# Performance work log

Hardware: AMD Instinct MI355X
Metric: run time of the kernel (lower is better)

## Reference

```python
import jax, jax.numpy as jnp
import numpy as np

B, N, D, Z, H = 256, 128, 256, 64, 128

def setup_inputs() -> dict:
    key = jax.random.key(0)
    ks = jax.random.split(key, 12)
    s = 0.02
    inp = {
        "h_obs": jax.random.normal(ks[0], (B, N, D), jnp.float32),
        "z": jax.random.normal(ks[1], (B, N, Z), jnp.float32),
        "start_pos": jax.random.normal(ks[2], (B, N, 2), jnp.float32),
        # input_proj: Linear(D+Z+2 -> H)
        "W_in": jax.random.normal(ks[3], (D + Z + 2, H), jnp.float32) * s,
        "b_in": jax.random.normal(ks[4], (H,), jnp.float32) * s,
        # GRUCell weights, PyTorch layout: [3H, H] rows ordered (r, z, n)
        "W_ih": jax.random.normal(ks[5], (3 * H, H), jnp.float32) * s,
        "b_ih": jax.random.normal(ks[6], (3 * H,), jnp.float32) * s,
        "W_hh": jax.random.normal(ks[7], (3 * H, H), jnp.float32) * s,
        "b_hh": jax.random.normal(ks[8], (3 * H,), jnp.float32) * s,
        # out_proj: Linear(H -> 2)
        "W_out": jax.random.normal(ks[9], (2, H), jnp.float32) * s,
        "b_out": jax.random.normal(ks[10], (2,), jnp.float32) * s,
        "pred_len": 30,
    }
    return inp

def _gru_cell(x, h, W_ih, b_ih, W_hh, b_hh):
    gi = x @ W_ih.T + b_ih            # [BN, 3H]
    gh = h @ W_hh.T + b_hh            # [BN, 3H]
    i_r, i_z, i_n = jnp.split(gi, 3, axis=-1)
    h_r, h_z, h_n = jnp.split(gh, 3, axis=-1)
    r = jax.nn.sigmoid(i_r + h_r)
    zg = jax.nn.sigmoid(i_z + h_z)
    n = jnp.tanh(i_n + r * h_n)
    return (1.0 - zg) * n + zg * h

def reference(h_obs, z, start_pos, W_in, b_in, W_ih, b_ih, W_hh, b_hh, W_out, b_out, pred_len):
    BN = B * N
    # h_obs and z are constant across steps: precompute their projection once.
    base = jnp.concatenate([h_obs, z], axis=-1).reshape(BN, D + Z)
    base_proj = base @ W_in[: D + Z] + b_in            # [BN, H]
    W_pos = W_in[D + Z:]                               # [2, H]

    state0 = jnp.zeros((BN, H), h_obs.dtype)
    pos0 = start_pos.reshape(BN, 2)

    def step(carry, _):
        state, pos = carry
        x = base_proj + pos @ W_pos                    # == input_proj(cat(h,z,pos))
        state = _gru_cell(x, state, W_ih, b_ih, W_hh, b_hh)
        delta = state @ W_out.T + b_out                # [BN, 2]
        pos = pos + delta
        return (state, pos), pos

    (_, _), traj = jax.lax.scan(step, (state0, pos0), None, length=pred_len)
    # traj: [T, BN, 2] -> [B, T, N, 2]
    return traj.reshape(pred_len, B, N, 2).transpose(1, 0, 2, 3)
```

## Files before the change

kernel.cpp:

```cpp
#include <hip/hip_runtime.h>
#include <hip/hip_bf16.h>


#define T_LEN 30
#define H_    128
#define G3_   384
#define KIN_  320

typedef float  f32x4 __attribute__((ext_vector_type(4)));
typedef __bf16 b16x8 __attribute__((ext_vector_type(8)));

#define MFMA16(a,b,c) __builtin_amdgcn_mfma_f32_16x16x32_bf16((a),(b),(c),0,0,0)

__device__ __forceinline__ float fast_sigmoid(float x){
  return __builtin_amdgcn_rcpf(1.0f + __builtin_amdgcn_exp2f(-1.4426950408889634f*x));
}
__device__ __forceinline__ float fast_tanh(float x){
  return 1.0f - 2.0f*__builtin_amdgcn_rcpf(1.0f + __builtin_amdgcn_exp2f(2.8853900817779268f*x));
}
__device__ __forceinline__ b16x8 pack8(float4 a, float4 b){
  b16x8 r;
  r[0]=(__bf16)a.x; r[1]=(__bf16)a.y; r[2]=(__bf16)a.z; r[3]=(__bf16)a.w;
  r[4]=(__bf16)b.x; r[5]=(__bf16)b.y; r[6]=(__bf16)b.z; r[7]=(__bf16)b.w;
  return r;
}

__global__ void prep_wc(const float* __restrict__ W_in, const float* __restrict__ W_ih,
                        __bf16* __restrict__ WcT){
  __shared__ float win[H_];
  int k = blockIdx.x;
  if (threadIdx.x < H_) win[threadIdx.x] = W_in[(size_t)k*H_ + threadIdx.x];
  __syncthreads();
  int j = threadIdx.x;
  const float* wr = W_ih + (size_t)j*H_;
  float s = 0.f;
  #pragma unroll 8
  for (int m=0;m<H_;m++) s += wr[m]*win[m];
  WcT[(size_t)j*KIN_ + k] = (__bf16)s;
}

__global__ void prep_vec(const float* __restrict__ W_in, const float* __restrict__ b_in,
                         const float* __restrict__ W_ih, const float* __restrict__ b_ih,
                         const float* __restrict__ b_hh,
                         float* __restrict__ cvec, float* __restrict__ P2G){
  int j = threadIdx.x;
  const float* wr = W_ih + (size_t)j*H_;
  float s  = b_ih[j] + (j < 2*H_ ? b_hh[j] : 0.f);
  float p0 = 0.f, p1 = 0.f;
  #pragma unroll 8
  for (int m=0;m<H_;m++){
    float w = wr[m];
    s  += b_in[m]*w;
    p0 += W_in[(size_t)KIN_*H_ + m]*w;
    p1 += W_in[(size_t)(KIN_+1)*H_ + m]*w;
  }
  cvec[j] = s; P2G[j] = p0; P2G[G3_ + j] = p1;
}

__global__ __launch_bounds__(512, 2)
void decoder(const float* __restrict__ h_obs, const float* __restrict__ zin,
             const float* __restrict__ start_pos,
             const float* __restrict__ W_hh, const float* __restrict__ b_hh,
             const float* __restrict__ W_out, const float* __restrict__ b_out,
             const __bf16* __restrict__ WcT, const float* __restrict__ cvec,
             const float* __restrict__ P2G, float* __restrict__ out)
{
  __shared__ __bf16 smraw[32*328];

  const int tid  = threadIdx.x;
  const int lane = tid & 63;
  const int w    = tid >> 6;
  const int l15  = lane & 15;
  const int lhi  = lane >> 4;
  const int R0   = blockIdx.x << 5;
  const int hcol = (w<<4) + l15;
  const int jr = hcol, jz = H_ + hcol, jn = 2*H_ + hcol;

  {
    const float4* src = reinterpret_cast<const float4*>(h_obs) + (size_t)R0*64;
    #pragma unroll
    for (int i=0;i<4;i++){
      int k = tid + (i<<9);
      float4 v = src[k];
      int r = k>>6, c = (k&63)<<2;
      __bf16* d = &smraw[r*328 + c];
      d[0]=(__bf16)v.x; d[1]=(__bf16)v.y; d[2]=(__bf16)v.z; d[3]=(__bf16)v.w;
    }
    const float4* srcz = reinterpret_cast<const float4*>(zin) + (size_t)R0*16;
    {
      int k = tid;
      float4 v = srcz[k];
      int r = k>>4, c = 256 + ((k&15)<<2);
      __bf16* d = &smraw[r*328 + c];
      d[0]=(__bf16)v.x; d[1]=(__bf16)v.y; d[2]=(__bf16)v.z; d[3]=(__bf16)v.w;
    }
  }
  __syncthreads();

  f32x4 G[3][2];
  {
    float cr = cvec[jr], cz = cvec[jz], cn = cvec[jn];
    G[0][0] = (f32x4){cr,cr,cr,cr}; G[0][1] = G[0][0];
    G[1][0] = (f32x4){cz,cz,cz,cz}; G[1][1] = G[1][0];
    G[2][0] = (f32x4){cn,cn,cn,cn}; G[2][1] = G[2][0];
    #pragma unroll 1
    for (int kk=0; kk<10; kk++){
      const int ko = (kk<<5) + (lhi<<3);
      b16x8 a0 = *reinterpret_cast<const b16x8*>(&smraw[(l15   )*328 + ko]);
      b16x8 a1 = *reinterpret_cast<const b16x8*>(&smraw[(16+l15)*328 + ko]);
      b16x8 br = *reinterpret_cast<const b16x8*>(WcT + (size_t)jr*KIN_ + ko);
      b16x8 bz = *reinterpret_cast<const b16x8*>(WcT + (size_t)jz*KIN_ + ko);
      b16x8 bn = *reinterpret_cast<const b16x8*>(WcT + (size_t)jn*KIN_ + ko);
      G[0][0] = MFMA16(a0, br, G[0][0]); G[0][1] = MFMA16(a1, br, G[0][1]);
      G[1][0] = MFMA16(a0, bz, G[1][0]); G[1][1] = MFMA16(a1, bz, G[1][1]);
      G[2][0] = MFMA16(a0, bn, G[2][0]); G[2][1] = MFMA16(a1, bn, G[2][1]);
    }
  }
  __syncthreads();

  b16x8 Bh[3][4];
  #pragma unroll
  for (int kk=0;kk<4;kk++){
    const int ko = (kk<<5) + (lhi<<3);
    { const float* p = W_hh + (size_t)jr*H_ + ko;
      Bh[0][kk] = pack8(*(const float4*)p, *(const float4*)(p+4)); }
    { const float* p = W_hh + (size_t)jz*H_ + ko;
      Bh[1][kk] = pack8(*(const float4*)p, *(const float4*)(p+4)); }
    { const float* p = W_hh + (size_t)jn*H_ + ko;
      Bh[2][kk] = pack8(*(const float4*)p, *(const float4*)(p+4)); }
  }
  const int oc = l15 & 1;
  b16x8 Bo[4];
  #pragma unroll
  for (int kk=0;kk<4;kk++){
    const float* p = W_out + (size_t)oc*H_ + (kk<<5) + (lhi<<3);
    Bo[kk] = pack8(*(const float4*)p, *(const float4*)(p+4));
  }
  const float pgr0 = P2G[jr], pgr1 = P2G[G3_+jr];
  const float pgz0 = P2G[jz], pgz1 = P2G[G3_+jz];
  const float pgn0 = P2G[jn], pgn1 = P2G[G3_+jn];
  const float bhn  = b_hh[2*H_ + hcol];
  const float bo   = b_out[oc];

  float posx[2][4], posy[2][4], st[2][4];
  #pragma unroll
  for (int m=0;m<2;m++)
    #pragma unroll
    for (int q=0;q<4;q++){
      int r = R0 + (m<<4) + (lhi<<2) + q;
      posx[m][q] = start_pos[2*r];
      posy[m][q] = start_pos[2*r+1];
    }

  #pragma unroll
  for (int m=0;m<2;m++)
    #pragma unroll
    for (int q=0;q<4;q++){
      float p0 = posx[m][q], p1 = posy[m][q];
      float rg = fast_sigmoid(G[0][m][q] + p0*pgr0 + p1*pgr1);
      float zg = fast_sigmoid(G[1][m][q] + p0*pgz0 + p1*pgz1);
      float nn = fast_tanh(fmaf(rg, bhn, G[2][m][q] + p0*pgn0 + p1*pgn1));
      float hnew = nn - zg*nn;
      st[m][q] = hnew;
      smraw[((m<<4)+(lhi<<2)+q)*152 + hcol] = (__bf16)hnew;
    }

  int cur = 0;
  #pragma unroll 1
  for (int t=1; t<T_LEN; ++t){
    __syncthreads();
    f32x4 acc00={0,0,0,0},acc01=acc00,acc10=acc00,acc11=acc00,acc20=acc00,acc21=acc00;
    f32x4 d0a=acc00, d1a=acc00;
    #pragma unroll
    for (int kk=0;kk<4;kk++){
      const int ko = (kk<<5)+(lhi<<3);
      b16x8 a0 = *reinterpret_cast<const b16x8*>(&smraw[cur*4864 + (l15   )*152 + ko]);
      b16x8 a1 = *reinterpret_cast<const b16x8*>(&smraw[cur*4864 + (16+l15)*152 + ko]);
      d0a   = MFMA16(a0, Bo[kk],   d0a);
      d1a   = MFMA16(a1, Bo[kk],   d1a);
      acc00 = MFMA16(a0, Bh[0][kk], acc00);
      acc01 = MFMA16(a1, Bh[0][kk], acc01);
      acc10 = MFMA16(a0, Bh[1][kk], acc10);
      acc11 = MFMA16(a1, Bh[1][kk], acc11);
      acc20 = MFMA16(a0, Bh[2][kk], acc20);
      acc21 = MFMA16(a1, Bh[2][kk], acc21);
    }
    #pragma unroll
    for (int m=0;m<2;m++)
      #pragma unroll
      for (int q=0;q<4;q++){
        float dme  = ((m==0)? d0a[q] : d1a[q]) + bo;
        float doth = __shfl_xor(dme, 1);
        posx[m][q] += (oc==0)? dme  : doth;
        posy[m][q] += (oc==0)? doth : dme;
      }
    if (w==0 && l15==0){
      #pragma unroll
      for (int m=0;m<2;m++)
        #pragma unroll
        for (int q=0;q<4;q++){
          int r  = R0 + (m<<4) + (lhi<<2) + q;
          int bb = r >> 7, n = r & 127;
          float2 v; v.x = posx[m][q]; v.y = posy[m][q];
          *reinterpret_cast<float2*>(out + (((size_t)(bb*T_LEN + (t-1))<<7) + n)*2) = v;
        }
    }
    const int nb = cur ^ 1;
    #pragma unroll
    for (int m=0;m<2;m++)
      #pragma unroll
      for (int q=0;q<4;q++){
        float p0 = posx[m][q], p1 = posy[m][q];
        float ar = (m==0)? acc00[q] : acc01[q];
        float az = (m==0)? acc10[q] : acc11[q];
        float an = (m==0)? acc20[q] : acc21[q];
        float rg = fast_sigmoid(ar + G[0][m][q] + p0*pgr0 + p1*pgr1);
        float zg = fast_sigmoid(az + G[1][m][q] + p0*pgz0 + p1*pgz1);
        float hn = an + bhn;
        float nn = fast_tanh(fmaf(rg, hn, G[2][m][q] + p0*pgn0 + p1*pgn1));
        float hnew = fmaf(zg, st[m][q] - nn, nn);
        st[m][q] = hnew;
        smraw[nb*4864 + ((m<<4)+(lhi<<2)+q)*152 + hcol] = (__bf16)hnew;
      }
    cur = nb;
  }

  __syncthreads();
  {
    f32x4 d0a={0,0,0,0}, d1a={0,0,0,0};
    #pragma unroll
    for (int kk=0;kk<4;kk++){
      const int ko = (kk<<5)+(lhi<<3);
      b16x8 a0 = *reinterpret_cast<const b16x8*>(&smraw[cur*4864 + (l15   )*152 + ko]);
      b16x8 a1 = *reinterpret_cast<const b16x8*>(&smraw[cur*4864 + (16+l15)*152 + ko]);
      d0a = MFMA16(a0, Bo[kk], d0a);
      d1a = MFMA16(a1, Bo[kk], d1a);
    }
    #pragma unroll
    for (int m=0;m<2;m++)
      #pragma unroll
      for (int q=0;q<4;q++){
        float dme  = ((m==0)? d0a[q] : d1a[q]) + bo;
        float doth = __shfl_xor(dme, 1);
        posx[m][q] += (oc==0)? dme  : doth;
        posy[m][q] += (oc==0)? doth : dme;
      }
    if (w==0 && l15==0){
      #pragma unroll
      for (int m=0;m<2;m++)
        #pragma unroll
        for (int q=0;q<4;q++){
          int r  = R0 + (m<<4) + (lhi<<2) + q;
          int bb = r >> 7, n = r & 127;
          float2 v; v.x = posx[m][q]; v.y = posy[m][q];
          *reinterpret_cast<float2*>(out + (((size_t)(bb*T_LEN + (T_LEN-1))<<7) + n)*2) = v;
        }
    }
  }
}

extern "C" void kernel_launch(void* const* d_in, const int* in_sizes, int n_in,
                              void* d_out, int out_size, void* d_ws, size_t ws_size,
                              hipStream_t stream) {
  const float* h_obs     = (const float*)d_in[0];
  const float* z         = (const float*)d_in[1];
  const float* start_pos = (const float*)d_in[2];
  const float* W_in      = (const float*)d_in[3];
  const float* b_in      = (const float*)d_in[4];
  const float* W_ih      = (const float*)d_in[5];
  const float* b_ih      = (const float*)d_in[6];
  const float* W_hh      = (const float*)d_in[7];
  const float* b_hh      = (const float*)d_in[8];
  const float* W_out     = (const float*)d_in[9];
  const float* b_out     = (const float*)d_in[10];

  __bf16* WcT = (__bf16*)d_ws;
  float*  cvec = (float*)((char*)d_ws + (size_t)G3_*KIN_*2);
  float*  P2G  = cvec + G3_;

  prep_wc <<<KIN_, G3_, 0, stream>>>(W_in, W_ih, WcT);
  prep_vec<<<1,    G3_, 0, stream>>>(W_in, b_in, W_ih, b_ih, b_hh, cvec, P2G);
  decoder <<<1024, 512, 0, stream>>>(h_obs, z, start_pos, W_hh, b_hh, W_out, b_out,
                                     WcT, cvec, P2G, (float*)d_out);
}
```

Measured before the change: 353.2 us.

## Process 64 rows per block, fold gate scales into weights, stage trajectory in LDS

Each block now handles 64 rows as two 32-row groups, which halves the grid and lets each weight fragment held in registers serve twice as many rows. The sigmoid/tanh exponent scales are folded into the precomputed weights, biases and W_hh, and the biases are used as MFMA initial accumulators, which removes per-element multiplies and adds from the recurrent loop. Per-step trajectory outputs are buffered in LDS and written out once at the end as coalesced stores instead of scattered float2 writes. In exchange the kernel needs more registers and LDS per block and has half as many blocks, which can lower occupancy and latency hiding.

```diff
diff --git a/kernel.cpp b/kernel.cpp
--- a/kernel.cpp
+++ b/kernel.cpp
@@ -6,22 +6,23 @@
 #define H_    128
 #define G3_   384
 #define KIN_  320
+#define S_    152
+#define HBYTES (64*S_*2)
+#define TRAJ_OFF (2*HBYTES)
+#define LDS_BYTES (TRAJ_OFF + T_LEN*64*2*4)
+
+#define SCL_RZ -1.44269504088896341f
+#define SCL_N   2.88539008177792681f
 
 typedef float  f32x4 __attribute__((ext_vector_type(4)));
 typedef __bf16 b16x8 __attribute__((ext_vector_type(8)));
 
 #define MFMA16(a,b,c) __builtin_amdgcn_mfma_f32_16x16x32_bf16((a),(b),(c),0,0,0)
 
-__device__ __forceinline__ float fast_sigmoid(float x){
-  return __builtin_amdgcn_rcpf(1.0f + __builtin_amdgcn_exp2f(-1.4426950408889634f*x));
-}
-__device__ __forceinline__ float fast_tanh(float x){
-  return 1.0f - 2.0f*__builtin_amdgcn_rcpf(1.0f + __builtin_amdgcn_exp2f(2.8853900817779268f*x));
-}
-__device__ __forceinline__ b16x8 pack8(float4 a, float4 b){
+__device__ __forceinline__ b16x8 pack8s(const float* p, float s){
   b16x8 r;
-  r[0]=(__bf16)a.x; r[1]=(__bf16)a.y; r[2]=(__bf16)a.z; r[3]=(__bf16)a.w;
-  r[4]=(__bf16)b.x; r[5]=(__bf16)b.y; r[6]=(__bf16)b.z; r[7]=(__bf16)b.w;
+  #pragma unroll
+  for (int i=0;i<8;i++) r[i] = (__bf16)(s*p[i]);
   return r;
 }
 
@@ -36,7 +37,8 @@
   float s = 0.f;
   #pragma unroll 8
   for (int m=0;m<H_;m++) s += wr[m]*win[m];
-  WcT[(size_t)j*KIN_ + k] = (__bf16)s;
+  float scl = (j < 2*H_) ? SCL_RZ : SCL_N;
+  WcT[(size_t)j*KIN_ + k] = (__bf16)(scl*s);
 }
 
 __global__ void prep_vec(const float* __restrict__ W_in, const float* __restrict__ b_in,
@@ -54,7 +56,8 @@
     p0 += W_in[(size_t)KIN_*H_ + m]*w;
     p1 += W_in[(size_t)(KIN_+1)*H_ + m]*w;
   }
-  cvec[j] = s; P2G[j] = p0; P2G[G3_ + j] = p1;
+  float scl = (j < 2*H_) ? SCL_RZ : SCL_N;
+  cvec[j] = scl*s; P2G[j] = scl*p0; P2G[G3_ + j] = scl*p1;
 }
 
 __global__ __launch_bounds__(512, 2)
@@ -65,196 +68,234 @@
              const __bf16* __restrict__ WcT, const float* __restrict__ cvec,
              const float* __restrict__ P2G, float* __restrict__ out)
 {
-  __shared__ __bf16 smraw[32*328];
+  __shared__ __align__(16) char lds[LDS_BYTES];
+  __bf16* hbuf = (__bf16*)lds;
+  float*  traj = (float*)(lds + TRAJ_OFF);
+  __bf16* stg  = (__bf16*)lds;
 
   const int tid  = threadIdx.x;
   const int lane = tid & 63;
   const int w    = tid >> 6;
   const int l15  = lane & 15;
   const int lhi  = lane >> 4;
-  const int R0   = blockIdx.x << 5;
+  const int R0   = blockIdx.x << 6;
   const int hcol = (w<<4) + l15;
   const int jr = hcol, jz = H_ + hcol, jn = 2*H_ + hcol;
+  const int oc = l15 & 1;
 
   {
     const float4* src = reinterpret_cast<const float4*>(h_obs) + (size_t)R0*64;
     #pragma unroll
-    for (int i=0;i<4;i++){
+    for (int i=0;i<8;i++){
       int k = tid + (i<<9);
       float4 v = src[k];
       int r = k>>6, c = (k&63)<<2;
-      __bf16* d = &smraw[r*328 + c];
+      __bf16* d = &stg[r*328 + c];
       d[0]=(__bf16)v.x; d[1]=(__bf16)v.y; d[2]=(__bf16)v.z; d[3]=(__bf16)v.w;
     }
     const float4* srcz = reinterpret_cast<const float4*>(zin) + (size_t)R0*16;
-    {
-      int k = tid;
+    #pragma unroll
+    for (int i=0;i<2;i++){
+      int k = tid + (i<<9);
       float4 v = srcz[k];
       int r = k>>4, c = 256 + ((k&15)<<2);
-      __bf16* d = &smraw[r*328 + c];
+      __bf16* d = &stg[r*328 + c];
       d[0]=(__bf16)v.x; d[1]=(__bf16)v.y; d[2]=(__bf16)v.z; d[3]=(__bf16)v.w;
     }
   }
   __syncthreads();
 
-  f32x4 G[3][2];
+  f32x4 G[2][3][2];
   {
     float cr = cvec[jr], cz = cvec[jz], cn = cvec[jn];
-    G[0][0] = (f32x4){cr,cr,cr,cr}; G[0][1] = G[0][0];
-    G[1][0] = (f32x4){cz,cz,cz,cz}; G[1][1] = G[1][0];
-    G[2][0] = (f32x4){cn,cn,cn,cn}; G[2][1] = G[2][0];
+    #pragma unroll
+    for (int g=0; g<2; g++){
+      G[g][0][0] = (f32x4){cr,cr,cr,cr}; G[g][0][1] = G[g][0][0];
+      G[g][1][0] = (f32x4){cz,cz,cz,cz}; G[g][1][1] = G[g][1][0];
+      G[g][2][0] = (f32x4){cn,cn,cn,cn}; G[g][2][1] = G[g][2][0];
+    }
     #pragma unroll 1
     for (int kk=0; kk<10; kk++){
       const int ko = (kk<<5) + (lhi<<3);
-      b16x8 a0 = *reinterpret_cast<const b16x8*>(&smraw[(l15   )*328 + ko]);
-      b16x8 a1 = *reinterpret_cast<const b16x8*>(&smraw[(16+l15)*328 + ko]);
       b16x8 br = *reinterpret_cast<const b16x8*>(WcT + (size_t)jr*KIN_ + ko);
       b16x8 bz = *reinterpret_cast<const b16x8*>(WcT + (size_t)jz*KIN_ + ko);
       b16x8 bn = *reinterpret_cast<const b16x8*>(WcT + (size_t)jn*KIN_ + ko);
-      G[0][0] = MFMA16(a0, br, G[0][0]); G[0][1] = MFMA16(a1, br, G[0][1]);
-      G[1][0] = MFMA16(a0, bz, G[1][0]); G[1][1] = MFMA16(a1, bz, G[1][1]);
-      G[2][0] = MFMA16(a0, bn, G[2][0]); G[2][1] = MFMA16(a1, bn, G[2][1]);
-    }
-  }
-  __syncthreads();
-
-  b16x8 Bh[3][4];
+      #pragma unroll
+      for (int g=0; g<2; g++){
+        b16x8 a0 = *reinterpret_cast<const b16x8*>(&stg[(g*32   +l15)*328 + ko]);
+        b16x8 a1 = *reinterpret_cast<const b16x8*>(&stg[(g*32+16+l15)*328 + ko]);
+        G[g][0][0] = MFMA16(a0, br, G[g][0][0]); G[g][0][1] = MFMA16(a1, br, G[g][0][1]);
+        G[g][1][0] = MFMA16(a0, bz, G[g][1][0]); G[g][1][1] = MFMA16(a1, bz, G[g][1][1]);
+        G[g][2][0] = MFMA16(a0, bn, G[g][2][0]); G[g][2][1] = MFMA16(a1, bn, G[g][2][1]);
+      }
+    }
+  }
+
+  b16x8 Bh[3][4], Bo[4];
   #pragma unroll
   for (int kk=0;kk<4;kk++){
     const int ko = (kk<<5) + (lhi<<3);
-    { const float* p = W_hh + (size_t)jr*H_ + ko;
-      Bh[0][kk] = pack8(*(const float4*)p, *(const float4*)(p+4)); }
-    { const float* p = W_hh + (size_t)jz*H_ + ko;
-      Bh[1][kk] = pack8(*(const float4*)p, *(const float4*)(p+4)); }
-    { const float* p = W_hh + (size_t)jn*H_ + ko;
-      Bh[2][kk] = pack8(*(const float4*)p, *(const float4*)(p+4)); }
-  }
-  const int oc = l15 & 1;
-  b16x8 Bo[4];
-  #pragma unroll
-  for (int kk=0;kk<4;kk++){
-    const float* p = W_out + (size_t)oc*H_ + (kk<<5) + (lhi<<3);
-    Bo[kk] = pack8(*(const float4*)p, *(const float4*)(p+4));
+    Bh[0][kk] = pack8s(W_hh + (size_t)jr*H_ + ko, SCL_RZ);
+    Bh[1][kk] = pack8s(W_hh + (size_t)jz*H_ + ko, SCL_RZ);
+    Bh[2][kk] = pack8s(W_hh + (size_t)jn*H_ + ko, SCL_N);
+    Bo[kk]    = pack8s(W_out + (size_t)oc*H_ + ko, 1.0f);
   }
   const float pgr0 = P2G[jr], pgr1 = P2G[G3_+jr];
   const float pgz0 = P2G[jz], pgz1 = P2G[G3_+jz];
   const float pgn0 = P2G[jn], pgn1 = P2G[G3_+jn];
-  const float bhn  = b_hh[2*H_ + hcol];
+  const float bhn  = SCL_N * b_hh[2*H_ + hcol];
   const float bo   = b_out[oc];
-
-  float posx[2][4], posy[2][4], st[2][4];
+  const f32x4 bovec  = (f32x4){bo,bo,bo,bo};
+  const f32x4 bhnvec = (f32x4){bhn,bhn,bhn,bhn};
+
+  float posx[2][2][4], posy[2][2][4], st[2][2][4];
   #pragma unroll
-  for (int m=0;m<2;m++)
-    #pragma unroll
-    for (int q=0;q<4;q++){
-      int r = R0 + (m<<4) + (lhi<<2) + q;
-      posx[m][q] = start_pos[2*r];
-      posy[m][q] = start_pos[2*r+1];
-    }
+  for (int g=0; g<2; g++)
+    #pragma unroll
+    for (int m=0;m<2;m++)
+      #pragma unroll
+      for (int q=0;q<4;q++){
+        int r = R0 + (g<<5) + (m<<4) + (lhi<<2) + q;
+        posx[g][m][q] = start_pos[2*r];
+        posy[g][m][q] = start_pos[2*r+1];
+      }
+
+  __syncthreads();
 
   #pragma unroll
-  for (int m=0;m<2;m++)
-    #pragma unroll
-    for (int q=0;q<4;q++){
-      float p0 = posx[m][q], p1 = posy[m][q];
-      float rg = fast_sigmoid(G[0][m][q] + p0*pgr0 + p1*pgr1);
-      float zg = fast_sigmoid(G[1][m][q] + p0*pgz0 + p1*pgz1);
-      float nn = fast_tanh(fmaf(rg, bhn, G[2][m][q] + p0*pgn0 + p1*pgn1));
-      float hnew = nn - zg*nn;
-      st[m][q] = hnew;
-      smraw[((m<<4)+(lhi<<2)+q)*152 + hcol] = (__bf16)hnew;
-    }
+  for (int g=0; g<2; g++)
+    #pragma unroll
+    for (int m=0;m<2;m++)
+      #pragma unroll
+      for (int q=0;q<4;q++){
+        float p0 = posx[g][m][q], p1 = posy[g][m][q];
+        float rg = __builtin_amdgcn_rcpf(1.f + __builtin_amdgcn_exp2f(
+                     fmaf(p1,pgr1, fmaf(p0,pgr0, G[g][0][m][q]))));
+        float zg = __builtin_amdgcn_rcpf(1.f + __builtin_amdgcn_exp2f(
+                     fmaf(p1,pgz1, fmaf(p0,pgz0, G[g][1][m][q]))));
+        float inn = fmaf(p1,pgn1, fmaf(p0,pgn0, G[g][2][m][q]));
+        float nn = fmaf(-2.f, __builtin_amdgcn_rcpf(1.f + __builtin_amdgcn_exp2f(
+                     fmaf(rg, bhn, inn))), 1.f);
+        float hnew = nn - zg*nn;
+        st[g][m][q] = hnew;
+        hbuf[((g<<5)+(m<<4)+(lhi<<2)+q)*S_ + hcol] = (__bf16)hnew;
+      }
+
+  const unsigned rdbA = (unsigned)(l15*(S_*2) + (lhi<<4));
+  const unsigned wrbA = (unsigned)((lhi<<2)*(S_*2) + hcol*2);
 
   int cur = 0;
   #pragma unroll 1
   for (int t=1; t<T_LEN; ++t){
     __syncthreads();
-    f32x4 acc00={0,0,0,0},acc01=acc00,acc10=acc00,acc11=acc00,acc20=acc00,acc21=acc00;
-    f32x4 d0a=acc00, d1a=acc00;
-    #pragma unroll
-    for (int kk=0;kk<4;kk++){
-      const int ko = (kk<<5)+(lhi<<3);
-      b16x8 a0 = *reinterpret_cast<const b16x8*>(&smraw[cur*4864 + (l15   )*152 + ko]);
-      b16x8 a1 = *reinterpret_cast<const b16x8*>(&smraw[cur*4864 + (16+l15)*152 + ko]);
-      d0a   = MFMA16(a0, Bo[kk],   d0a);
-      d1a   = MFMA16(a1, Bo[kk],   d1a);
-      acc00 = MFMA16(a0, Bh[0][kk], acc00);
-      acc01 = MFMA16(a1, Bh[0][kk], acc01);
-      acc10 = MFMA16(a0, Bh[1][kk], acc10);
-      acc11 = MFMA16(a1, Bh[1][kk], acc11);
-      acc20 = MFMA16(a0, Bh[2][kk], acc20);
-      acc21 = MFMA16(a1, Bh[2][kk], acc21);
-    }
-    #pragma unroll
-    for (int m=0;m<2;m++)
-      #pragma unroll
-      for (int q=0;q<4;q++){
-        float dme  = ((m==0)? d0a[q] : d1a[q]) + bo;
-        float doth = __shfl_xor(dme, 1);
-        posx[m][q] += (oc==0)? dme  : doth;
-        posy[m][q] += (oc==0)? doth : dme;
-      }
-    if (w==0 && l15==0){
+    const char* rb = lds + cur*HBYTES;
+    char*       wb = lds + (cur^1)*HBYTES;
+
+    #pragma unroll
+    for (int g=0; g<2; g++){
+      const unsigned go = g*(32*S_*2);
+      f32x4 ar0, ar1, az0, az1, an0, an1, d0, d1;
+      #pragma unroll
+      for (int kk=0;kk<4;kk++){
+        b16x8 a0 = *reinterpret_cast<const b16x8*>(rb + go + rdbA + kk*64);
+        b16x8 a1 = *reinterpret_cast<const b16x8*>(rb + go + rdbA + 16*S_*2 + kk*64);
+        if (kk==0){
+          d0  = MFMA16(a0, Bo[0],   bovec);  d1  = MFMA16(a1, Bo[0],   bovec);
+          ar0 = MFMA16(a0, Bh[0][0], G[g][0][0]); ar1 = MFMA16(a1, Bh[0][0], G[g][0][1]);
+          az0 = MFMA16(a0, Bh[1][0], G[g][1][0]); az1 = MFMA16(a1, Bh[1][0], G[g][1][1]);
+          an0 = MFMA16(a0, Bh[2][0], bhnvec);     an1 = MFMA16(a1, Bh[2][0], bhnvec);
+        } else {
+          d0  = MFMA16(a0, Bo[kk],   d0);  d1  = MFMA16(a1, Bo[kk],   d1);
+          ar0 = MFMA16(a0, Bh[0][kk], ar0); ar1 = MFMA16(a1, Bh[0][kk], ar1);
+          az0 = MFMA16(a0, Bh[1][kk], az0); az1 = MFMA16(a1, Bh[1][kk], az1);
+          an0 = MFMA16(a0, Bh[2][kk], an0); an1 = MFMA16(a1, Bh[2][kk], an1);
+        }
+      }
       #pragma unroll
       for (int m=0;m<2;m++)
         #pragma unroll
         for (int q=0;q<4;q++){
-          int r  = R0 + (m<<4) + (lhi<<2) + q;
-          int bb = r >> 7, n = r & 127;
-          float2 v; v.x = posx[m][q]; v.y = posy[m][q];
-          *reinterpret_cast<float2*>(out + (((size_t)(bb*T_LEN + (t-1))<<7) + n)*2) = v;
+          float dme  = (m==0)? d0[q] : d1[q];
+          float doth = __shfl_xor(dme, 1);
+          posx[g][m][q] += oc ? doth : dme;
+          posy[g][m][q] += oc ? dme  : doth;
         }
-    }
-    const int nb = cur ^ 1;
-    #pragma unroll
-    for (int m=0;m<2;m++)
-      #pragma unroll
-      for (int q=0;q<4;q++){
-        float p0 = posx[m][q], p1 = posy[m][q];
-        float ar = (m==0)? acc00[q] : acc01[q];
-        float az = (m==0)? acc10[q] : acc11[q];
-        float an = (m==0)? acc20[q] : acc21[q];
-        float rg = fast_sigmoid(ar + G[0][m][q] + p0*pgr0 + p1*pgr1);
-        float zg = fast_sigmoid(az + G[1][m][q] + p0*pgz0 + p1*pgz1);
-        float hn = an + bhn;
-        float nn = fast_tanh(fmaf(rg, hn, G[2][m][q] + p0*pgn0 + p1*pgn1));
-        float hnew = fmaf(zg, st[m][q] - nn, nn);
-        st[m][q] = hnew;
-        smraw[nb*4864 + ((m<<4)+(lhi<<2)+q)*152 + hcol] = (__bf16)hnew;
-      }
-    cur = nb;
+      if (w==g && l15==0){
+        #pragma unroll
+        for (int m=0;m<2;m++)
+          #pragma unroll
+          for (int q=0;q<4;q++){
+            int rr = (g<<5) + (m<<4) + (lhi<<2) + q;
+            float2 v; v.x = posx[g][m][q]; v.y = posy[g][m][q];
+            *reinterpret_cast<float2*>(&traj[(t-1)*128 + rr*2]) = v;
+          }
+      }
+      #pragma unroll
+      for (int m=0;m<2;m++)
+        #pragma unroll
+        for (int q=0;q<4;q++){
+          float p0 = posx[g][m][q], p1 = posy[g][m][q];
+          float ar = (m==0)? ar0[q] : ar1[q];
+          float az = (m==0)? az0[q] : az1[q];
+          float hn = (m==0)? an0[q] : an1[q];
+          float rg = __builtin_amdgcn_rcpf(1.f + __builtin_amdgcn_exp2f(
+                       fmaf(p1,pgr1, fmaf(p0,pgr0, ar))));
+          float zg = __builtin_amdgcn_rcpf(1.f + __builtin_amdgcn_exp2f(
+                       fmaf(p1,pgz1, fmaf(p0,pgz0, az))));
+          float inn = fmaf(p1,pgn1, fmaf(p0,pgn0, G[g][2][m][q]));
+          float nn = fmaf(-2.f, __builtin_amdgcn_rcpf(1.f + __builtin_amdgcn_exp2f(
+                       fmaf(rg, hn, inn))), 1.f);
+          float hnew = fmaf(zg, st[g][m][q] - nn, nn);
+          st[g][m][q] = hnew;
+          *reinterpret_cast<__bf16*>(wb + go + wrbA + (m*16+q)*(S_*2)) = (__bf16)hnew;
+        }
+    }
+    cur ^= 1;
   }
 
   __syncthreads();
   {
-    f32x4 d0a={0,0,0,0}, d1a={0,0,0,0};
-    #pragma unroll
-    for (int kk=0;kk<4;kk++){
-      const int ko = (kk<<5)+(lhi<<3);
-      b16x8 a0 = *reinterpret_cast<const b16x8*>(&smraw[cur*4864 + (l15   )*152 + ko]);
-      b16x8 a1 = *reinterpret_cast<const b16x8*>(&smraw[cur*4864 + (16+l15)*152 + ko]);
-      d0a = MFMA16(a0, Bo[kk], d0a);
-      d1a = MFMA16(a1, Bo[kk], d1a);
-    }
-    #pragma unroll
-    for (int m=0;m<2;m++)
-      #pragma unroll
-      for (int q=0;q<4;q++){
-        float dme  = ((m==0)? d0a[q] : d1a[q]) + bo;
-        float doth = __shfl_xor(dme, 1);
-        posx[m][q] += (oc==0)? dme  : doth;
-        posy[m][q] += (oc==0)? doth : dme;
-      }
-    if (w==0 && l15==0){
+    const char* rb = lds + cur*HBYTES;
+    #pragma unroll
+    for (int g=0; g<2; g++){
+      const unsigned go = g*(32*S_*2);
+      f32x4 d0, d1;
+      #pragma unroll
+      for (int kk=0;kk<4;kk++){
+        b16x8 a0 = *reinterpret_cast<const b16x8*>(rb + go + rdbA + kk*64);
+        b16x8 a1 = *reinterpret_cast<const b16x8*>(rb + go + rdbA + 16*S_*2 + kk*64);
+        if (kk==0){ d0 = MFMA16(a0, Bo[0], bovec); d1 = MFMA16(a1, Bo[0], bovec); }
+        else      { d0 = MFMA16(a0, Bo[kk], d0);   d1 = MFMA16(a1, Bo[kk], d1);   }
+      }
       #pragma unroll
       for (int m=0;m<2;m++)
         #pragma unroll
         for (int q=0;q<4;q++){
-          int r  = R0 + (m<<4) + (lhi<<2) + q;
-          int bb = r >> 7, n = r & 127;
-          float2 v; v.x = posx[m][q]; v.y = posy[m][q];
-          *reinterpret_cast<float2*>(out + (((size_t)(bb*T_LEN + (T_LEN-1))<<7) + n)*2) = v;
+          float dme  = (m==0)? d0[q] : d1[q];
+          float doth = __shfl_xor(dme, 1);
+          posx[g][m][q] += oc ? doth : dme;
+          posy[g][m][q] += oc ? dme  : doth;
         }
+      if (w==g && l15==0){
+        #pragma unroll
+        for (int m=0;m<2;m++)
+          #pragma unroll
+          for (int q=0;q<4;q++){
+            int rr = (g<<5) + (m<<4) + (lhi<<2) + q;
+            float2 v; v.x = posx[g][m][q]; v.y = posy[g][m][q];
+            *reinterpret_cast<float2*>(&traj[(T_LEN-1)*128 + rr*2]) = v;
+          }
+      }
+    }
+  }
+
+  __syncthreads();
+  {
+    const size_t ob  = ((size_t)(R0>>7)*T_LEN)<<8;
+    const int    n02 = (R0 & 127)<<1;
+    for (int i=tid; i<T_LEN*128; i+=512){
+      int tt = i>>7, j = i&127;
+      out[ob + (size_t)tt*256 + n02 + j] = traj[i];
     }
   }
 }
@@ -274,12 +315,12 @@
   const float* W_out     = (const float*)d_in[9];
   const float* b_out     = (const float*)d_in[10];
 
-  __bf16* WcT = (__bf16*)d_ws;
+  __bf16* WcT  = (__bf16*)d_ws;
   float*  cvec = (float*)((char*)d_ws + (size_t)G3_*KIN_*2);
   float*  P2G  = cvec + G3_;
 
   prep_wc <<<KIN_, G3_, 0, stream>>>(W_in, W_ih, WcT);
   prep_vec<<<1,    G3_, 0, stream>>>(W_in, b_in, W_ih, b_ih, b_hh, cvec, P2G);
-  decoder <<<1024, 512, 0, stream>>>(h_obs, z, start_pos, W_hh, b_hh, W_out, b_out,
-                                     WcT, cvec, P2G, (float*)d_out);
-}
+  decoder <<<512, 512, 0, stream>>>(h_obs, z, start_pos, W_hh, b_hh, W_out, b_out,
+                                    WcT, cvec, P2G, (float*)d_out);
+}
```

New measurement: 309.8 us. -12.3%, faster.
